# Performance work log

Hardware: AMD Instinct MI355X
Metric: run time of the kernel (lower is better)

Reference implementation:

```python
import jax, jax.numpy as jnp
import numpy as np

B, CIN, MID, COUT, H, W = 4, 256, 128, 64, 128, 128
WS, HEADS = 8, 8
HD = MID // HEADS          # head dim = 16
N = WS * WS                # tokens per window = 64


def conv2d(x, w, pad=0, groups=1):
    return jax.lax.conv_general_dilated(
        x, w, (1, 1), ((pad, pad), (pad, pad)),
        feature_group_count=groups,
        dimension_numbers=('NCHW', 'OIHW', 'NCHW'))


def bn(x, g, b):  # eval-mode BatchNorm folded to per-channel affine
    return x * g[None, :, None, None] + b[None, :, None, None]


def setup_inputs() -> dict:
    key = jax.random.key(0)
    ks = jax.random.split(key, 32)
    nrm = lambda i, sh, s: jax.random.normal(ks[i], sh, jnp.float32) * s
    return {
        'x': nrm(0, (B, CIN, H, W), 1.0),
        'conv_w': nrm(1, (MID, CIN, 3, 3), 0.03),
        'bn1_g': 1.0 + nrm(2, (MID,), 0.05), 'bn1_b': nrm(3, (MID,), 0.05),
        'qkv_w': nrm(4, (3 * MID, MID, 1, 1), 0.05),
        'loc1_w': nrm(5, (MID, MID, 3, 3), 0.03),
        'loc1_g': 1.0 + nrm(6, (MID,), 0.05), 'loc1_b': nrm(7, (MID,), 0.05),
        'loc2_w': nrm(8, (MID, MID, 1, 1), 0.05),
        'loc2_g': 1.0 + nrm(9, (MID,), 0.05), 'loc2_b': nrm(10, (MID,), 0.05),
        'rel_table': nrm(11, ((2 * WS - 1) ** 2, HEADS), 0.02),
        'cw_w': nrm(12, (1, 2, 7, 7), 0.1),
        'cw_g': 1.0 + nrm(13, (1,), 0.05), 'cw_b': nrm(14, (1,), 0.05),
        'hc_w': nrm(15, (1, 2, 7, 7), 0.1),
        'hc_g': 1.0 + nrm(16, (1,), 0.05), 'hc_b': nrm(17, (1,), 0.05),
        'hw_w': nrm(18, (1, 2, 7, 7), 0.1),
        'hw_g': 1.0 + nrm(19, (1,), 0.05), 'hw_b': nrm(20, (1,), 0.05),
        'proj_dw': nrm(21, (MID, 1, WS, WS), 0.05),
        'proj_g': 1.0 + nrm(22, (MID,), 0.05), 'proj_b': nrm(23, (MID,), 0.05),
        'proj_pw': nrm(24, (MID, MID, 1, 1), 0.05),
        'up_w': nrm(25, (COUT, MID, 3, 3), 0.03),
    }


def _rel_pos_index():
    coords = np.stack(np.meshgrid(np.arange(WS), np.arange(WS), indexing='ij')).reshape(2, -1)
    rel = (coords[:, :, None] - coords[:, None, :]).transpose(1, 2, 0) + (WS - 1)
    return (rel[:, :, 0] * (2 * WS - 1) + rel[:, :, 1]).reshape(-1)  # [N*N]


def reference(x, conv_w, bn1_g, bn1_b, qkv_w, loc1_w, loc1_g, loc1_b,
              loc2_w, loc2_g, loc2_b, rel_table, cw_w, cw_g, cw_b,
              hc_w, hc_g, hc_b, hw_w, hw_g, hw_b,
              proj_dw, proj_g, proj_b, proj_pw, up_w):
    # DecoderBlock: conv -> BN -> ReLU
    h = jax.nn.relu(bn(conv2d(x, conv_w, pad=1), bn1_g, bn1_b))  # [B,MID,H,W]

    # GlobalLocalAttention
    local = bn(conv2d(h, loc2_w), loc2_g, loc2_b) + bn(conv2d(h, loc1_w, pad=1), loc1_g, loc1_b)

    # windowed qkv (H,W divisible by WS, no pad needed)
    hh, ww = H // WS, W // WS
    qkv = conv2d(h, qkv_w)  # [B, 3*MID, H, W]
    qkv = qkv.reshape(B, 3, HEADS, HD, hh, WS, ww, WS)
    qkv = qkv.transpose(1, 0, 4, 6, 2, 5, 7, 3).reshape(3, B * hh * ww, HEADS, N, HD)
    q, k, v = qkv[0], qkv[1], qkv[2]

    dots = jnp.einsum('bhnd,bhmd->bhnm', q, k) * (HD ** -0.5)  # [Bw,HEADS,N,N]
    bias = rel_table[jnp.asarray(_rel_pos_index())].reshape(N, N, HEADS).transpose(2, 0, 1)
    dots = dots + bias[None]

    # TripletAttention on dots treated as (B', C'=HEADS, H'=N, W'=N)
    def gate(t, w, g, b):
        z = jnp.concatenate([t.max(1, keepdims=True), t.mean(1, keepdims=True)], 1)  # ZPool
        return t * jax.nn.sigmoid(bn(conv2d(z, w, pad=3), g, b))

    d1 = gate(dots.transpose(0, 2, 1, 3), cw_w, cw_g, cw_b).transpose(0, 2, 1, 3)
    d2 = gate(dots.transpose(0, 3, 2, 1), hc_w, hc_g, hc_b).transpose(0, 3, 2, 1)
    d3 = gate(dots, hw_w, hw_g, hw_b)
    dots = (d1 + d2 + d3) / 3.0

    attn = jax.nn.softmax(dots, axis=-1)
    o = jnp.einsum('bhnm,bhmd->bhnd', attn, v)
    o = o.reshape(B, hh, ww, HEADS, WS, WS, HD).transpose(0, 3, 6, 1, 4, 2, 5).reshape(B, MID, H, W)

    # avg+max pooled sigmoid gates (kernel==stride==WS//2, exact reshape pooling)
    kp = WS // 2
    aw = o.reshape(B, MID, H // kp, kp, W)
    Fw = jax.nn.sigmoid(aw.mean(3) + aw.max(3))          # [B,MID,H/4,W]
    ah = o.reshape(B, MID, H, W // kp, kp)
    Fh = jax.nn.sigmoid(ah.mean(4) + ah.max(4))          # [B,MID,H,W/4]
    gmat = jnp.einsum('bchk,bckw->bchw', Fh, Fw)         # [B,MID,H,W]

    out = o * gmat + local
    out = jnp.pad(out, ((0, 0), (0, 0), (0, 1), (0, 1)), mode='reflect')  # pad_out
    # SeparableConvBN proj: depthwise k=WS pad=3 -> BN -> 1x1
    out = conv2d(out, proj_dw, pad=3, groups=MID)
    out = conv2d(bn(out, proj_g, proj_b), proj_pw)
    out = out[:, :, :H, :W]

    # upsample: ConvTranspose2d(k=3, s=2, p=1, op=1) as dilated conv
    up = jax.lax.conv_general_dilated(
        out, up_w, (1, 1), ((1, 2), (1, 2)), lhs_dilation=(2, 2),
        dimension_numbers=('NCHW', 'OIHW', 'NCHW'))  # [B,COUT,2H,2W]
    return up
```

## Files before the change

### kernel.cpp

```cpp
#include <hip/hip_runtime.h>
#include <hip/hip_bf16.h>

typedef __hip_bfloat16 bf16;
typedef __attribute__((ext_vector_type(8))) short short8;
typedef __attribute__((ext_vector_type(4))) float f32x4;

#define DEV __device__ __forceinline__
DEV float b2f(bf16 v){ return __bfloat162float(v); }
DEV bf16 f2b(float v){ return __float2bfloat16(v); }
DEV short f2bs(float v){ union{ bf16 b; short s; } u; u.b = __float2bfloat16(v); return u.s; }
DEV float s2f(short s){ union{ short s; bf16 b; } u; u.s = s; return __bfloat162float(u.b); }
DEV float sigm(float x){ return 1.f/(1.f + expf(-x)); }

#define BB 4
#define CIN 256
#define MID 128
#define COUT 64
#define HH 128
#define WW 128
#define WS 8
#define HEADS 8
#define HD 16
#define NTOK 64
#define NWIN 1024

#define SLOT(row,cq) ((cq) ^ (((row)>>1)&3))

static const size_t OFF_H     = 0;
static const size_t OFF_LOCAL = 33554432;
static const size_t OFF_Q     = 67108864;
static const size_t OFF_K     = 83886080;
static const size_t OFF_V     = 100663296;
static const size_t OFF_DOTS  = 117440512;
static const size_t OFF_Z1    = 184549376;
static const size_t OFF_Z2    = 186646528;
static const size_t OFF_Z3    = 188743680;
static const size_t OFF_G1    = 205520896;
static const size_t OFF_G2    = 207618048;
static const size_t OFF_G3    = 209715200;
static const size_t OFF_HT    = OFF_DOTS + 34078720;

__global__ __launch_bounds__(256) void k_wrep(const float* __restrict__ w, short* __restrict__ w2){
  int i = blockIdx.x*256 + threadIdx.x;
  int ci = i & 255, co = (i >> 8) & 127, kk = i >> 15;
  w2[i] = f2bs(w[(co*256 + ci)*9 + kk]);
}

__global__ void k_xzero(short* __restrict__ xT){
  int t = blockIdx.x*256 + threadIdx.x;
  int ci = t & 255, side = (t >> 8) & 1, row = t >> 9;
  int cpad = side ? 129 : 0;
  xT[((size_t)row*130 + cpad)*256 + ci] = 0;
}

__global__ __launch_bounds__(256) void k_xrep(const float* __restrict__ x, short* __restrict__ xT){
  const int blk = blockIdx.x;
  const int cgrp = blk & 1, cig = (blk >> 1) & 7, r = (blk >> 4) & 127, b = blk >> 11;
  const int c0 = cgrp*64, ci0 = cig*32;
  __shared__ float lds[32][65];
  const int t = threadIdx.x;
  for (int i = t; i < 2048; i += 256){
    int lci = i >> 6, c = i & 63;
    lds[lci][c] = x[((size_t)(b*256 + ci0 + lci)*128 + r)*128 + c0 + c];
  }
  __syncthreads();
  for (int i = t; i < 2048; i += 256){
    int lci = i & 31, cc = i >> 5;
    xT[((size_t)(b*128 + r)*130 + c0 + cc + 1)*256 + ci0 + lci] = f2bs(lds[lci][cc]);
  }
}

__global__ __launch_bounds__(256) void k_conv1m(const short* __restrict__ xT, const short* __restrict__ w2,
      const float* __restrict__ gg, const float* __restrict__ bb, short* __restrict__ hT){
  int blk = blockIdx.x;
  blk = (blk & 7)*64 + (blk >> 3);
  const int cg = blk & 1, y2 = (blk >> 1) & 63, b = blk >> 7;
  const int t = threadIdx.x, lane = t & 63, wave = t >> 6;
  const int quad = lane >> 4, l15 = lane & 15;
  const int r = wave >> 1, x0w = (wave & 1)*64;
  __shared__ __align__(16) short smem[22784];
  short* as = smem;
  short* bs = smem + 16640;
  f32x4 acc[4][4];
  #pragma unroll
  for (int i = 0; i < 4; ++i)
    #pragma unroll
    for (int j = 0; j < 4; ++j) acc[i][j] = (f32x4){0.f,0.f,0.f,0.f};
  for (int ch = 0; ch < 8; ++ch){
    const int ci0 = ch*32;
    #pragma unroll 1
    for (int ky = 0; ky < 3; ++ky){
      __syncthreads();
      if (ky == 0){
        for (int i = t; i < 2080; i += 256){
          int sr = i / 520, j = i - sr*520;
          int col = j >> 2, cq = j & 3;
          int g = 2*y2 - 1 + sr;
          uint4 val = {0,0,0,0};
          if ((unsigned)g < 128u)
            val = *(const uint4*)&xT[((size_t)(b*128+g)*130 + col)*256 + ci0 + cq*8];
          *(uint4*)&as[((sr*130 + col)*4 + SLOT(col,cq))*8] = val;
        }
      }
      for (int i = t; i < 768; i += 256){
        int rr = i >> 2, cq = i & 3;
        int kk = ky*3 + (rr >> 6), co_l = rr & 63;
        *(uint4*)&bs[(rr*4 + SLOT(rr,cq))*8] =
          *(const uint4*)&w2[((size_t)(kk*128 + cg*64 + co_l))*256 + ci0 + cq*8];
      }
      __syncthreads();
      const int sr = r + ky;
      #pragma unroll
      for (int kx = 0; kx < 3; ++kx){
        short8 af[4], bf[4];
        #pragma unroll
        for (int mt = 0; mt < 4; ++mt){
          int col = x0w + mt*16 + l15 + kx;
          af[mt] = *(const short8*)&as[((sr*130 + col)*4 + SLOT(col,quad))*8];
        }
        #pragma unroll
        for (int nt = 0; nt < 4; ++nt){
          int rr = kx*64 + nt*16 + l15;
          bf[nt] = *(const short8*)&bs[(rr*4 + SLOT(rr,quad))*8];
        }
        #pragma unroll
        for (int mt = 0; mt < 4; ++mt)
          #pragma unroll
          for (int nt = 0; nt < 4; ++nt)
            acc[mt][nt] = __builtin_amdgcn_mfma_f32_16x16x32_bf16(af[mt], bf[nt], acc[mt][nt], 0, 0, 0);
      }
    }
  }
  __syncthreads();
  short* tb = smem;
  #pragma unroll
  for (int nt = 0; nt < 4; ++nt){
    int cl = nt*16 + l15, co = cg*64 + cl;
    float g = gg[co], bia = bb[co];
    #pragma unroll
    for (int mt = 0; mt < 4; ++mt){
      int xb = x0w + mt*16 + quad*4;
      #pragma unroll
      for (int r2 = 0; r2 < 4; ++r2)
        tb[(r*128 + xb + r2)*72 + cl] = f2bs(fmaxf(acc[mt][nt][r2]*g + bia, 0.f));
    }
  }
  __syncthreads();
  for (int i = t; i < 2048; i += 256){
    int rr = i >> 10, xx = (i >> 3) & 127, c8 = i & 7;
    *(uint4*)&hT[((size_t)(b*128 + 2*y2 + rr)*130 + xx + 1)*128 + cg*64 + c8*8] =
      *(const uint4*)&tb[(rr*128 + xx)*72 + c8*8];
  }
}

__global__ void k_hzero(short* __restrict__ hT){
  int t = blockIdx.x*256 + threadIdx.x;
  int ci = t & 127, side = (t >> 7) & 1, row = t >> 8;
  int cpad = side ? 129 : 0;
  hT[((size_t)row*130 + cpad)*128 + ci] = 0;
}

__global__ __launch_bounds__(256) void k_lwrep(const float* __restrict__ w1, const float* __restrict__ g1,
      const float* __restrict__ w2, const float* __restrict__ g2, short* __restrict__ wloc){
  int i = blockIdx.x*256 + threadIdx.x;
  int ci = i & 127, row = (i >> 7) % 384, ky = i / 49152;
  int kx = row >> 7, co = row & 127;
  float v = w1[(co*128 + ci)*9 + ky*3 + kx] * g1[co];
  if (ky == 1 && kx == 1) v += w2[co*128 + ci] * g2[co];
  wloc[i] = f2bs(v);
}

__global__ __launch_bounds__(256) void k_localm(const short* __restrict__ hT, const short* __restrict__ wloc,
      const float* __restrict__ b1, const float* __restrict__ b2, float* __restrict__ out){
  int blk = blockIdx.x;
  blk = (blk & 7)*64 + (blk >> 3);
  const int cg = blk & 1, y2 = (blk >> 1) & 63, b = blk >> 7;
  const int t = threadIdx.x, lane = t & 63, wave = t >> 6;
  const int quad = lane >> 4, l15 = lane & 15;
  const int r = wave >> 1, x0w = (wave & 1)*64;
  __shared__ __align__(16) short smem2[22784];
  short* as = smem2;
  short* bs = smem2 + 16640;
  f32x4 acc[4][4];
  #pragma unroll
  for (int i = 0; i < 4; ++i)
    #pragma unroll
    for (int j = 0; j < 4; ++j) acc[i][j] = (f32x4){0.f,0.f,0.f,0.f};
  for (int ch = 0; ch < 4; ++ch){
    const int ci0 = ch*32;
    #pragma unroll 1
    for (int ky = 0; ky < 3; ++ky){
      __syncthreads();
      if (ky == 0){
        for (int i = t; i < 2080; i += 256){
          int sr = i / 520, j = i - sr*520;
          int col = j >> 2, cq = j & 3;
          int g = 2*y2 - 1 + sr;
          uint4 val = {0,0,0,0};
          if ((unsigned)g < 128u)
            val = *(const uint4*)&hT[((size_t)(b*128+g)*130 + col)*128 + ci0 + cq*8];
          *(uint4*)&as[((sr*130 + col)*4 + SLOT(col,cq))*8] = val;
        }
      }
      for (int i = t; i < 768; i += 256){
        int rr = i >> 2, cq = i & 3;
        int kk = ky*3 + (rr >> 6), co_l = rr & 63;
        *(uint4*)&bs[(rr*4 + SLOT(rr,cq))*8] =
          *(const uint4*)&wloc[((size_t)(kk*128 + cg*64 + co_l))*128 + ci0 + cq*8];
      }
      __syncthreads();
      const int sr = r + ky;
      #pragma unroll
      for (int kx = 0; kx < 3; ++kx){
        short8 af[4], bf[4];
        #pragma unroll
        for (int mt = 0; mt < 4; ++mt){
          int col = x0w + mt*16 + l15 + kx;
          af[mt] = *(const short8*)&as[((sr*130 + col)*4 + SLOT(col,quad))*8];
        }
        #pragma unroll
        for (int nt = 0; nt < 4; ++nt){
          int rr = kx*64 + nt*16 + l15;
          bf[nt] = *(const short8*)&bs[(rr*4 + SLOT(rr,quad))*8];
        }
        #pragma unroll
        for (int mt = 0; mt < 4; ++mt)
          #pragma unroll
          for (int nt = 0; nt < 4; ++nt)
            acc[mt][nt] = __builtin_amdgcn_mfma_f32_16x16x32_bf16(af[mt], bf[nt], acc[mt][nt], 0, 0, 0);
      }
    }
  }
  const int Y = 2*y2 + r;
  #pragma unroll
  for (int nt = 0; nt < 4; ++nt){
    int co = cg*64 + nt*16 + l15;
    float bia = b1[co] + b2[co];
    #pragma unroll
    for (int mt = 0; mt < 4; ++mt){
      int xb = x0w + mt*16 + quad*4;
      float4 o4;
      o4.x = acc[mt][nt][0] + bia;
      o4.y = acc[mt][nt][1] + bia;
      o4.z = acc[mt][nt][2] + bia;
      o4.w = acc[mt][nt][3] + bia;
      *(float4*)&out[((size_t)(b*128 + co)*128 + Y)*128 + xb] = o4;
    }
  }
}

__global__ __launch_bounds__(256) void k_wqkvrep(const float* __restrict__ w, short* __restrict__ wqkv){
  int i = blockIdx.x*256 + threadIdx.x;
  wqkv[i] = f2bs(w[i]);
}

__global__ __launch_bounds__(256) void k_qkvm(const short* __restrict__ hT, const short* __restrict__ wqkv,
      bf16* __restrict__ q, bf16* __restrict__ k, bf16* __restrict__ v){
  const int blk = blockIdx.x, ocg = blockIdx.y;
  const int b = blk >> 7, y = blk & 127;
  const int t = threadIdx.x, lane = t & 63, wave = t >> 6;
  const int quad = lane >> 4, l15 = lane & 15;
  const int m0 = (wave >> 1)*64, n0 = (wave & 1)*64;
  __shared__ __align__(16) short asq[4096];
  __shared__ __align__(16) short bsq[4096];
  const short* xrow = hT + ((size_t)(b*128 + y)*130 + 1)*128;
  const short* wk   = wqkv + (size_t)ocg*128*128;
  f32x4 acc[4][4];
  #pragma unroll
  for (int i = 0; i < 4; ++i)
    #pragma unroll
    for (int j = 0; j < 4; ++j) acc[i][j] = (f32x4){0.f,0.f,0.f,0.f};
  for (int ch = 0; ch < 4; ++ch){
    const int ci0 = ch*32;
    __syncthreads();
    for (int i = t; i < 512; i += 256){
      int col = i >> 2, cq = i & 3;
      *(uint4*)&asq[(col*4 + SLOT(col,cq))*8] = *(const uint4*)&xrow[col*128 + ci0 + cq*8];
    }
    for (int i = t; i < 512; i += 256){
      int rr = i >> 2, cq = i & 3;
      *(uint4*)&bsq[(rr*4 + SLOT(rr,cq))*8] = *(const uint4*)&wk[rr*128 + ci0 + cq*8];
    }
    __syncthreads();
    short8 af[4], bf[4];
    #pragma unroll
    for (int mt = 0; mt < 4; ++mt){
      int row = m0 + mt*16 + l15;
      af[mt] = *(const short8*)&asq[(row*4 + SLOT(row,quad))*8];
    }
    #pragma unroll
    for (int nt = 0; nt < 4; ++nt){
      int row = n0 + nt*16 + l15;
      bf[nt] = *(const short8*)&bsq[(row*4 + SLOT(row,quad))*8];
    }
    #pragma unroll
    for (int mt = 0; mt < 4; ++mt)
      #pragma unroll
      for (int nt = 0; nt < 4; ++nt)
        acc[mt][nt] = __builtin_amdgcn_mfma_f32_16x16x32_bf16(af[mt], bf[nt], acc[mt][nt], 0, 0, 0);
  }
  bf16* dst = (ocg == 0) ? q : (ocg == 1) ? k : v;
  const int iy = y & 7, hy = y >> 3;
  #pragma unroll
  for (int nt = 0; nt < 4; ++nt){
    int co = n0 + nt*16 + l15;
    int head = co >> 4, d = co & 15;
    #pragma unroll
    for (int mt = 0; mt < 4; ++mt){
      int xb = m0 + mt*16 + quad*4;
      #pragma unroll
      for (int rr = 0; rr < 4; ++rr){
        int x = xb + rr;
        int bw = b*256 + hy*16 + (x >> 3);
        int n = iy*8 + (x & 7);
        dst[((size_t)(bw*8+head)*64 + n)*16 + d] = f2b(acc[mt][nt][rr]);
      }
    }
  }
}

__global__ __launch_bounds__(256) void k_dots(const bf16* __restrict__ q, const bf16* __restrict__ kk,
      const float* __restrict__ rel, bf16* __restrict__ dots){
  const int bw = blockIdx.x, hd = blockIdx.y;
  __shared__ bf16 qs[64][16], ks[64][16];
  const int t = threadIdx.x;
  const size_t base = (size_t)(bw*8+hd)*1024;
  for (int i = t; i < 1024; i += 256){ qs[i>>4][i&15] = q[base + i]; ks[i>>4][i&15] = kk[base + i]; }
  __syncthreads();
  const int n = t >> 2, jm = t & 3;
  float qr[16];
  #pragma unroll
  for (int d = 0; d < 16; ++d) qr[d] = b2f(qs[n][d]);
  const int ny = n >> 3, nx = n & 7;
  for (int mm = 0; mm < 16; ++mm){
    int m = jm*16 + mm;
    float a = 0.f;
    #pragma unroll
    for (int d = 0; d < 16; ++d) a += qr[d]*b2f(ks[m][d]);
    int my = m >> 3, mx = m & 7;
    int ridx = (ny - my + 7)*15 + (nx - mx + 7);
    float bias = rel[ridx*8 + hd];
    dots[base*4 + (size_t)n*64 + m] = f2b(a*0.25f + bias);
  }
}

__global__ __launch_bounds__(256) void k_zall(const bf16* __restrict__ dots,
      bf16* __restrict__ z1, bf16* __restrict__ z2, bf16* __restrict__ z3){
  const int bw = blockIdx.x;
  const int t = threadIdx.x;
  const int q4 = t >> 2, j4 = t & 3;
  __shared__ float sd[64][65];
  float mx3[16], sm3[16];
  #pragma unroll
  for (int i = 0; i < 16; ++i){ mx3[i] = -1e30f; sm3[i] = 0.f; }
  const short* dp = (const short*)dots + (size_t)bw*32768;
  for (int hd = 0; hd < 8; ++hd){
    __syncthreads();
    const short* p = dp + (size_t)hd*4096;
    #pragma unroll
    for (int g = 0; g < 2; ++g){
      short8 s8 = *(const short8*)&p[t*16 + g*8];
      #pragma unroll
      for (int j = 0; j < 8; ++j){
        float vv = s2f(s8[j]);
        sd[q4][j4*16 + g*8 + j] = vv;
        mx3[g*8+j] = fmaxf(mx3[g*8+j], vv);
        sm3[g*8+j] += vv;
      }
    }
    __syncthreads();
    float mx = -1e30f, sm = 0.f;
    #pragma unroll
    for (int m = 0; m < 16; ++m){
      float vv = sd[q4][j4*16 + m];
      mx = fmaxf(mx, vv); sm += vv;
    }
    mx = fmaxf(mx, __shfl_xor(mx, 1, 4));
    mx = fmaxf(mx, __shfl_xor(mx, 2, 4));
    sm += __shfl_xor(sm, 1, 4);
    sm += __shfl_xor(sm, 2, 4);
    if (j4 == 0){
      z2[(size_t)bw*1024 + q4*8 + hd]       = f2b(mx);
      z2[(size_t)bw*1024 + 512 + q4*8 + hd] = f2b(sm*(1.f/64.f));
    }
    float mxc = -1e30f, smc = 0.f;
    #pragma unroll
    for (int nn = 0; nn < 16; ++nn){
      float vv = sd[j4*16 + nn][q4];
      mxc = fmaxf(mxc, vv); smc += vv;
    }
    mxc = fmaxf(mxc, __shfl_xor(mxc, 1, 4));
    mxc = fmaxf(mxc, __shfl_xor(mxc, 2, 4));
    smc += __shfl_xor(smc, 1, 4);
    smc += __shfl_xor(smc, 2, 4);
    if (j4 == 0){
      z1[(size_t)bw*1024 + hd*64 + q4]       = f2b(mxc);
      z1[(size_t)bw*1024 + 512 + hd*64 + q4] = f2b(smc*(1.f/64.f));
    }
  }
  short* zp = (short*)z3 + (size_t)bw*8192;
  short8 o0, o1, p0, p1;
  #pragma unroll
  for (int j = 0; j < 8; ++j){
    o0[j] = f2bs(mx3[j]);        o1[j] = f2bs(mx3[8+j]);
    p0[j] = f2bs(sm3[j]*0.125f); p1[j] = f2bs(sm3[8+j]*0.125f);
  }
  *(short8*)&zp[t*16]          = o0;
  *(short8*)&zp[t*16 + 8]      = o1;
  *(short8*)&zp[4096 + t*16]   = p0;
  *(short8*)&zp[4096 + t*16+8] = p1;
}

__global__ __launch_bounds__(256) void k_gate(const bf16* __restrict__ z, const float* __restrict__ w,
      const float* __restrict__ gg, const float* __restrict__ bb, float* __restrict__ G, int R, int C){
  __shared__ float wsm[98];
  const int t = threadIdx.x;
  if (t < 98) wsm[t] = w[t];
  __syncthreads();
  const int bw = blockIdx.x;
  int p = blockIdx.y*256 + t; if (p >= R*C) return;
  int y = p / C, x = p - y*C;
  float acc = 0.f;
  for (int c = 0; c < 2; ++c)
    for (int ky = 0; ky < 7; ++ky){
      int iy = y + ky - 3; if ((unsigned)iy >= (unsigned)R) continue;
      for (int kx = 0; kx < 7; ++kx){
        int ix = x + kx - 3; if ((unsigned)ix >= (unsigned)C) continue;
        acc += b2f(z[((size_t)(bw*2+c)*R + iy)*C + ix]) * wsm[c*49 + ky*7 + kx];
      }
    }
  G[(size_t)bw*R*C + p] = sigm(acc*gg[0] + bb[0]);
}

__global__ __launch_bounds__(256) void k_gate3(const bf16* __restrict__ z, const float* __restrict__ w,
      const float* __restrict__ gg, const float* __restrict__ bb, float* __restrict__ G){
  const int bw = blockIdx.x;
  __shared__ float pad[2][70][72];
  __shared__ float wsm[98];
  const int t = threadIdx.x;
  if (t < 98) wsm[t] = w[t];
  for (int i = t; i < 2*70*70; i += 256){
    int c = i / 4900, r = i % 4900;
    int py = r / 70, px = r % 70;
    int y = py - 3, x = px - 3;
    float v = 0.f;
    if ((unsigned)y < 64u && (unsigned)x < 64u)
      v = b2f(z[(size_t)bw*8192 + c*4096 + y*64 + x]);
    pad[c][py][px] = v;
  }
  __syncthreads();
  const int tx = t & 15, ty = t >> 4;
  const int x0 = tx*4, y0 = ty*4;
  float acc[4][4] = {};
  #pragma unroll
  for (int c = 0; c < 2; ++c){
    float wr[49];
    #pragma unroll
    for (int kk = 0; kk < 49; ++kk) wr[kk] = wsm[c*49 + kk];
    #pragma unroll
    for (int iy = 0; iy < 10; ++iy){
      float row[10];
      #pragma unroll
      for (int j = 0; j < 10; ++j) row[j] = pad[c][y0+iy][x0+j];
      #pragma unroll
      for (int dy = 0; dy < 4; ++dy){
        const int ky = iy - dy;
        if (ky < 0 || ky > 6) continue;
        #pragma unroll
        for (int kx = 0; kx < 7; ++kx){
          float wv = wr[ky*7 + kx];
          #pragma unroll
          for (int dx = 0; dx < 4; ++dx)
            acc[dy][dx] += wv * row[dx + kx];
        }
      }
    }
  }
  float g0 = gg[0], b0 = bb[0];
  #pragma unroll
  for (int dy = 0; dy < 4; ++dy){
    float4 o4;
    o4.x = sigm(acc[dy][0]*g0 + b0);
    o4.y = sigm(acc[dy][1]*g0 + b0);
    o4.z = sigm(acc[dy][2]*g0 + b0);
    o4.w = sigm(acc[dy][3]*g0 + b0);
    *(float4*)&G[(size_t)bw*4096 + (y0+dy)*64 + x0] = o4;
  }
}

__global__ __launch_bounds__(256) void k_attn(const bf16* __restrict__ dots, const float* __restrict__ G1,
      const float* __restrict__ G2, const float* __restrict__ G3, const bf16* __restrict__ v,
      float* __restrict__ o){
  const int bw = blockIdx.x, hd = blockIdx.y;
  const int b = bw >> 8, wy = (bw >> 4) & 15, wx = bw & 15;
  __shared__ float attn[64][65];
  __shared__ bf16 vs[64][16];
  __shared__ float invTot[64];
  const int t = threadIdx.x;
  for (int i = t; i < 1024; i += 256) vs[i>>4][i&15] = v[(size_t)(bw*8+hd)*1024 + i];
  const int n = t >> 2, j = t & 3;
  float g2v = G2[(size_t)bw*512 + n*8 + hd];
  const bf16* dp = dots + ((size_t)(bw*8+hd)*64 + n)*64 + j*16;
  const float* g1p = G1 + (size_t)bw*512 + hd*64 + j*16;
  const float* g3p = G3 + (size_t)bw*4096 + n*64 + j*16;
  float e[16]; float mx = -1e30f;
  #pragma unroll
  for (int m = 0; m < 16; ++m){
    float dv = b2f(dp[m]) * ((g1p[m] + g2v + g3p[m]) * (1.f/3.f));
    e[m] = dv; mx = fmaxf(mx, dv);
  }
  mx = fmaxf(mx, __shfl_xor(mx, 1, 4));
  mx = fmaxf(mx, __shfl_xor(mx, 2, 4));
  float s = 0.f;
  #pragma unroll
  for (int m = 0; m < 16; ++m){ float ev = expf(e[m]-mx); e[m] = ev; s += ev; }
  s += __shfl_xor(s, 1, 4);
  s += __shfl_xor(s, 2, 4);
  #pragma unroll
  for (int m = 0; m < 16; ++m) attn[n][j*16+m] = e[m];
  if (j == 0) invTot[n] = 1.f/s;
  __syncthreads();
  const int dg = j;
  float acc[4] = {0.f,0.f,0.f,0.f};
  for (int m = 0; m < 64; ++m){
    float a = attn[n][m];
    #pragma unroll
    for (int dd = 0; dd < 4; ++dd) acc[dd] += a * b2f(vs[m][dg*4+dd]);
  }
  float it = invTot[n];
  int y = wy*8 + (n>>3), x = wx*8 + (n&7);
  #pragma unroll
  for (int dd = 0; dd < 4; ++dd){
    int c = hd*16 + dg*4 + dd;
    o[((size_t)(b*128+c)*128 + y)*128 + x] = acc[dd]*it;
  }
}

__global__ void k_fw(const float* __restrict__ o, float* __restrict__ Fw){
  int t = blockIdx.x*256 + threadIdx.x; if (t >= 4*128*32*128) return;
  int x = t & 127, kk = (t>>7) & 31, bc = t >> 12;
  const float* p = o + ((size_t)bc*128 + kk*4)*128 + x;
  float mx = -1e30f, sm = 0.f;
  #pragma unroll
  for (int r = 0; r < 4; ++r){ float v = p[r*128]; mx = fmaxf(mx,v); sm += v; }
  Fw[t] = sigm(sm*0.25f + mx);
}
__global__ void k_fh(const float* __restrict__ o, float* __restrict__ Fh){
  int t = blockIdx.x*256 + threadIdx.x; if (t >= 4*128*128*32) return;
  int kk = t & 31, y = (t>>5) & 127, bc = t >> 12;
  const float* p = o + ((size_t)bc*128 + y)*128 + kk*4;
  float mx = -1e30f, sm = 0.f;
  #pragma unroll
  for (int r = 0; r < 4; ++r){ float v = p[r]; mx = fmaxf(mx,v); sm += v; }
  Fh[t] = sigm(sm*0.25f + mx);
}

__global__ __launch_bounds__(256) void k_comb(const float* __restrict__ o, const float* __restrict__ Fh,
      const float* __restrict__ Fw, const float* __restrict__ local, float* __restrict__ comb){
  const int bc = blockIdx.x;
  __shared__ float fh[128][33];
  __shared__ float fw[32][129];
  const int t = threadIdx.x;
  for (int i = t; i < 4096; i += 256) fh[i>>5][i&31]  = Fh[(size_t)bc*4096 + i];
  for (int i = t; i < 4096; i += 256) fw[i>>7][i&127] = Fw[(size_t)bc*4096 + i];
  __syncthreads();
  for (int i = t; i < 16384; i += 256){
    int y = i >> 7, x = i & 127;
    float g = 0.f;
    #pragma unroll
    for (int kk = 0; kk < 32; ++kk) g += fh[y][kk]*fw[kk][x];
    size_t idx = (size_t)bc*16384 + i;
    comb[idx] = o[idx]*g + local[idx];
  }
}

__global__ __launch_bounds__(256) void k_dw(const float* __restrict__ comb, const float* __restrict__ dw,
      const float* __restrict__ gg, const float* __restrict__ bb, float* __restrict__ out){
  const int bz = blockIdx.y;
  const int oy0 = blockIdx.x*16;
  const int c = bz & 127;
  __shared__ float xs[23][136];
  __shared__ float wsm[64];
  const int t = threadIdx.x;
  if (t < 64) wsm[t] = dw[c*64 + t];
  for (int i = t; i < 23*135; i += 256){
    int py = i / 135, px = i - py*135;
    int gy = oy0 + py - 3, gx = px - 3;
    float v = 0.f;
    if (gy >= 0 && gy <= 128 && gx >= 0 && gx <= 128){
      int yy = (gy==128)?126:gy, xx = (gx==128)?126:gx;
      v = comb[((size_t)bz*128 + yy)*128 + xx];
    }
    xs[py][px] = v;
  }
  __syncthreads();
  const int tx = t & 31, ty = t >> 5;
  const int x0 = tx*4, y0 = ty*2;
  float acc[2][4] = {};
  #pragma unroll
  for (int iy = 0; iy < 9; ++iy){
    float row[12];
    *(float4*)&row[0] = *(const float4*)&xs[y0+iy][x0];
    *(float4*)&row[4] = *(const float4*)&xs[y0+iy][x0+4];
    *(float4*)&row[8] = *(const float4*)&xs[y0+iy][x0+8];
    #pragma unroll
    for (int dy = 0; dy < 2; ++dy){
      const int ky = iy - dy;
      if (ky < 0 || ky > 7) continue;
      #pragma unroll
      for (int kx = 0; kx < 8; ++kx){
        float wv = wsm[ky*8 + kx];
        #pragma unroll
        for (int dx = 0; dx < 4; ++dx)
          acc[dy][dx] += wv * row[dx + kx];
      }
    }
  }
  float g = gg[c], bi = bb[c];
  #pragma unroll
  for (int dy = 0; dy < 2; ++dy){
    float4 o4;
    o4.x = acc[dy][0]*g + bi;
    o4.y = acc[dy][1]*g + bi;
    o4.z = acc[dy][2]*g + bi;
    o4.w = acc[dy][3]*g + bi;
    *(float4*)&out[((size_t)bz*128 + oy0 + y0 + dy)*128 + x0] = o4;
  }
}

__global__ void k_omzero(short* __restrict__ omT){
  int t = blockIdx.x*256 + threadIdx.x;
  int ci = t & 127, side = (t >> 7) & 1, row = t >> 8;
  int cpad = side ? 129 : 0;
  omT[((size_t)row*130 + cpad)*128 + ci] = 0;
}

__global__ __launch_bounds__(256) void k_uwrep(const float* __restrict__ w, short* __restrict__ wup){
  int i = blockIdx.x*256 + threadIdx.x;
  int ci = i & 127, co = (i >> 7) & 63, tap = i >> 13;
  wup[i] = f2bs(w[(co*128 + ci)*9 + tap]);
}

__global__ __launch_bounds__(256) void k_pw(const float* __restrict__ p1, const float* __restrict__ w,
      short* __restrict__ omT){
  const int pt = blockIdx.x, cb = blockIdx.y;
  const int P0 = pt*64; const int b = P0 >> 14; const int rem0 = P0 & 16383;
  const int y = rem0 >> 7, x0 = rem0 & 127;
  __shared__ float xsm[128][65];
  __shared__ float wsm[64][129];
  const int tx = threadIdx.x, ty = threadIdx.y, t = ty*16+tx;
  for (int i = t; i < 128*64; i += 256){
    int ci = i >> 6, p = i & 63;
    xsm[ci][p] = p1[(size_t)(b*128+ci)*16384 + rem0 + p];
  }
  for (int i = t; i < 64*128; i += 256){
    int co = i >> 7, ci = i & 127;
    wsm[co][ci] = w[(cb*64+co)*128 + ci];
  }
  __syncthreads();
  float acc[4][4] = {};
  for (int ci = 0; ci < 128; ++ci){
    float hv[4], wv[4];
    #pragma unroll
    for (int jj = 0; jj < 4; ++jj) hv[jj] = xsm[ci][jj*16+tx];
    #pragma unroll
    for (int ii = 0; ii < 4; ++ii) wv[ii] = wsm[ii*16+ty][ci];
    #pragma unroll
    for (int ii = 0; ii < 4; ++ii)
      #pragma unroll
      for (int jj = 0; jj < 4; ++jj) acc[ii][jj] += wv[ii]*hv[jj];
  }
  __syncthreads();
  float* pt_t = &xsm[0][0];
  #pragma unroll
  for (int ii = 0; ii < 4; ++ii)
    #pragma unroll
    for (int jj = 0; jj < 4; ++jj)
      pt_t[(jj*16+tx)*65 + ii*16+ty] = acc[ii][jj];
  __syncthreads();
  for (int i = t; i < 4096; i += 256){
    int px = i >> 6, co_l = i & 63;
    omT[((size_t)(b*128 + y)*130 + x0 + px + 1)*128 + cb*64 + co_l] = f2bs(pt_t[px*65 + co_l]);
  }
}

__global__ __launch_bounds__(256) void k_upm(const short* __restrict__ omT, const short* __restrict__ wup,
      float* __restrict__ out){
  int blk = blockIdx.x;
  blk = (blk & 7)*64 + (blk >> 3);
  const int b = blk >> 7, y = blk & 127;
  const int t = threadIdx.x, lane = t & 63, wave = t >> 6;
  const int quad = lane >> 4, l15 = lane & 15;
  const int m0w = wave*32;
  __shared__ __align__(16) char smem[53504];
  short* asp = (short*)smem;
  short* bsp = (short*)(smem + 16640);
  float* ptile = (float*)smem;
  const int PAR[9] = {3,2,3, 1,0,1, 3,2,3};
  const int ROW[9] = {0,0,0, 0,0,0, 1,1,1};
  const int SHF[9] = {0,0,1, 0,0,1, 0,0,1};
  f32x4 acc[4][2][4];
  #pragma unroll
  for (int p = 0; p < 4; ++p)
    #pragma unroll
    for (int mt = 0; mt < 2; ++mt)
      #pragma unroll
      for (int nt = 0; nt < 4; ++nt) acc[p][mt][nt] = (f32x4){0.f,0.f,0.f,0.f};
  for (int ch = 0; ch < 4; ++ch){
    const int ci0 = ch*32;
    __syncthreads();
    for (int i = t; i < 1040; i += 256){
      int rw = (i >= 520), j = i - rw*520;
      int col = j >> 2, cq = j & 3;
      int row = rw*130 + col;
      uint4 val = {0,0,0,0};
      if (y + rw < 128)
        val = *(const uint4*)&omT[((size_t)(b*128 + y + rw)*130 + col)*128 + ci0 + cq*8];
      *(uint4*)&asp[(row*4 + SLOT(row,cq))*8] = val;
    }
    for (int i = t; i < 2304; i += 256){
      int rr = i >> 2, cq = i & 3;
      *(uint4*)&bsp[(rr*4 + SLOT(rr,cq))*8] = *(const uint4*)&wup[rr*128 + ci0 + cq*8];
    }
    __syncthreads();
    #pragma unroll
    for (int k = 0; k < 9; ++k){
      const int pr = PAR[k], rw = ROW[k], sh = SHF[k];
      if (rw && y == 127) continue;
      short8 af[2], bf[4];
      #pragma unroll
      for (int mt = 0; mt < 2; ++mt){
        int row = rw*130 + m0w + mt*16 + l15 + 1 + sh;
        af[mt] = *(const short8*)&asp[(row*4 + SLOT(row,quad))*8];
      }
      #pragma unroll
      for (int nt = 0; nt < 4; ++nt){
        int row = k*64 + nt*16 + l15;
        bf[nt] = *(const short8*)&bsp[(row*4 + SLOT(row,quad))*8];
      }
      #pragma unroll
      for (int mt = 0; mt < 2; ++mt)
        #pragma unroll
        for (int nt = 0; nt < 4; ++nt)
          acc[pr][mt][nt] = __builtin_amdgcn_mfma_f32_16x16x32_bf16(af[mt], bf[nt], acc[pr][mt][nt], 0, 0, 0);
    }
  }
  #pragma unroll
  for (int p = 0; p < 4; ++p){
    __syncthreads();
    #pragma unroll
    for (int mt = 0; mt < 2; ++mt)
      #pragma unroll
      for (int nt = 0; nt < 4; ++nt){
        int co = nt*16 + l15;
        int xb = m0w + mt*16 + quad*4;
        #pragma unroll
        for (int r = 0; r < 4; ++r)
          ptile[co*132 + xb + r] = acc[p][mt][nt][r];
      }
    __syncthreads();
    int py = p >> 1, px = p & 1;
    int Y = 2*y + py;
    for (int i = t; i < 8192; i += 256){
      int co = i >> 7, xx = i & 127;
      out[((size_t)(b*64 + co)*256 + Y)*256 + 2*xx + px] = ptile[co*132 + xx];
    }
  }
}

extern "C" void kernel_launch(void* const* d_in, const int* in_sizes, int n_in,
                              void* d_out, int out_size, void* d_ws, size_t ws_size,
                              hipStream_t stream) {
  const float* x       = (const float*)d_in[0];
  const float* conv_w  = (const float*)d_in[1];
  const float* bn1_g   = (const float*)d_in[2];
  const float* bn1_b   = (const float*)d_in[3];
  const float* qkv_w   = (const float*)d_in[4];
  const float* loc1_w  = (const float*)d_in[5];
  const float* loc1_g  = (const float*)d_in[6];
  const float* loc1_b  = (const float*)d_in[7];
  const float* loc2_w  = (const float*)d_in[8];
  const float* loc2_g  = (const float*)d_in[9];
  const float* loc2_b  = (const float*)d_in[10];
  const float* rel_t   = (const float*)d_in[11];
  const float* cw_w    = (const float*)d_in[12];
  const float* cw_g    = (const float*)d_in[13];
  const float* cw_b    = (const float*)d_in[14];
  const float* hc_w    = (const float*)d_in[15];
  const float* hc_g    = (const float*)d_in[16];
  const float* hc_b    = (const float*)d_in[17];
  const float* hw_w    = (const float*)d_in[18];
  const float* hw_g    = (const float*)d_in[19];
  const float* hw_b    = (const float*)d_in[20];
  const float* proj_dw = (const float*)d_in[21];
  const float* proj_g  = (const float*)d_in[22];
  const float* proj_b  = (const float*)d_in[23];
  const float* proj_pw = (const float*)d_in[24];
  const float* up_w    = (const float*)d_in[25];

  char* ws = (char*)d_ws;
  float* local  = (float*)(ws + OFF_LOCAL);
  bf16*  q      = (bf16*)(ws + OFF_Q);
  bf16*  k      = (bf16*)(ws + OFF_K);
  bf16*  v      = (bf16*)(ws + OFF_V);
  bf16*  dots   = (bf16*)(ws + OFF_DOTS);
  bf16*  z1     = (bf16*)(ws + OFF_Z1);
  bf16*  z2     = (bf16*)(ws + OFF_Z2);
  bf16*  z3     = (bf16*)(ws + OFF_Z3);
  float* G1     = (float*)(ws + OFF_G1);
  float* G2     = (float*)(ws + OFF_G2);
  float* G3     = (float*)(ws + OFF_G3);
  short* xT     = (short*)(ws + OFF_DOTS);
  short* hT     = (short*)(ws + OFF_HT);
  short* w2bf   = (short*)(ws + OFF_Z1);
  short* wloc   = (short*)(ws + OFF_Z2);
  short* wqkv   = (short*)(ws + OFF_Z3);
  short* omT    = (short*)(ws + OFF_DOTS);
  short* wup    = (short*)(ws + OFF_Z1);
  float* o_img  = (float*)(ws + OFF_Q);
  float* Fh     = (float*)(ws + OFF_DOTS);
  float* Fw     = (float*)(ws + OFF_DOTS + 8388608);
  float* comb   = (float*)(ws + OFF_H);
  float* proj1  = (float*)(ws + OFF_LOCAL);
  float* outp   = (float*)d_out;

  dim3 blk2(16,16);
  k_wrep <<<1152, 256, 0, stream>>>(conv_w, w2bf);
  k_xzero<<<1024, 256, 0, stream>>>(xT);
  k_xrep <<<8192, 256, 0, stream>>>(x, xT);
  k_hzero<<<512, 256, 0, stream>>>(hT);
  k_conv1m<<<512, 256, 0, stream>>>(xT, w2bf, bn1_g, bn1_b, hT);
  k_lwrep<<<576, 256, 0, stream>>>(loc1_w, loc1_g, loc2_w, loc2_g, wloc);
  k_localm<<<512, 256, 0, stream>>>(hT, wloc, loc1_b, loc2_b, local);
  k_wqkvrep<<<192, 256, 0, stream>>>(qkv_w, wqkv);
  k_qkvm <<<dim3(512,3), 256, 0, stream>>>(hT, wqkv, q, k, v);
  k_dots <<<dim3(NWIN,8), 256, 0, stream>>>(q, k, rel_t, dots);
  k_zall <<<NWIN, 256, 0, stream>>>(dots, z1, z2, z3);
  k_gate <<<dim3(NWIN,2),  256, 0, stream>>>(z1, cw_w, cw_g, cw_b, G1, 8, 64);
  k_gate <<<dim3(NWIN,2),  256, 0, stream>>>(z2, hc_w, hc_g, hc_b, G2, 64, 8);
  k_gate3<<<NWIN, 256, 0, stream>>>(z3, hw_w, hw_g, hw_b, G3);
  k_attn <<<dim3(NWIN,8), 256, 0, stream>>>(dots, G1, G2, G3, v, o_img);
  k_fw   <<<8192, 256, 0, stream>>>(o_img, Fw);
  k_fh   <<<8192, 256, 0, stream>>>(o_img, Fh);
  k_comb <<<512, 256, 0, stream>>>(o_img, Fh, Fw, local, comb);
  k_dw   <<<dim3(8, BB*128), 256, 0, stream>>>(comb, proj_dw, proj_g, proj_b, proj1);
  k_omzero<<<512, 256, 0, stream>>>(omT);
  k_uwrep<<<288, 256, 0, stream>>>(up_w, wup);
  k_pw   <<<dim3(1024,2), blk2, 0, stream>>>(proj1, proj_pw, omT);
  k_upm  <<<512, 256, 0, stream>>>(omT, wup, outp);
}
```

Baseline: 643.1 us.

## Retile 3x3 convs to 4-row blocks with register prefetch; vectorize dots and attention LDS

The two 3x3 MFMA conv kernels now use 512-thread blocks covering 4 output rows. They prefetch the next input chunk and weight slices into registers while the current slice is computed, which is meant to hide global-load latency and cut redundant halo loads. The k_dots and k_attn kernels switch to 16-byte vectorized global/LDS loads and stores, with XOR-swizzled shared layouts for k and v to avoid bank conflicts. The trade-offs are higher register and LDS use, which may lower occupancy, and half as many conv blocks.

```diff
diff --git a/kernel.cpp b/kernel.cpp
--- a/kernel.cpp
+++ b/kernel.cpp
@@ -70,86 +70,135 @@
   }
 }
 
-__global__ __launch_bounds__(256) void k_conv1m(const short* __restrict__ xT, const short* __restrict__ w2,
+__global__ __launch_bounds__(512, 2) void k_conv1m(const short* __restrict__ xT, const short* __restrict__ w2,
       const float* __restrict__ gg, const float* __restrict__ bb, short* __restrict__ hT){
   int blk = blockIdx.x;
-  blk = (blk & 7)*64 + (blk >> 3);
-  const int cg = blk & 1, y2 = (blk >> 1) & 63, b = blk >> 7;
+  blk = (blk & 7)*32 + (blk >> 3);
+  const int cg = blk & 1, y4 = (blk >> 1) & 31, b = blk >> 6;
   const int t = threadIdx.x, lane = t & 63, wave = t >> 6;
   const int quad = lane >> 4, l15 = lane & 15;
-  const int r = wave >> 1, x0w = (wave & 1)*64;
-  __shared__ __align__(16) short smem[22784];
+  const int row = wave >> 1, xh = wave & 1;
+  const int x0w = xh*64;
+  __shared__ __align__(16) short smem[31104];
   short* as = smem;
-  short* bs = smem + 16640;
+  short* bs = smem + 24960;
+  uint4 areg[7], breg[2];
   f32x4 acc[4][4];
   #pragma unroll
   for (int i = 0; i < 4; ++i)
     #pragma unroll
     for (int j = 0; j < 4; ++j) acc[i][j] = (f32x4){0.f,0.f,0.f,0.f};
+
+  auto loadA = [&](int ch){
+    const int ci0 = ch*32;
+    #pragma unroll
+    for (int j = 0; j < 7; ++j){
+      int i = t + j*512;
+      uint4 val = {0,0,0,0};
+      if (j < 6 || i < 3120){
+        int sr = i / 520, jj = i - sr*520;
+        int col = jj >> 2, cq = jj & 3;
+        int g = y4*4 - 1 + sr;
+        if ((unsigned)g < 128u)
+          val = *(const uint4*)&xT[((size_t)(b*128+g)*130 + col)*256 + ci0 + cq*8];
+      }
+      areg[j] = val;
+    }
+  };
+  auto writeA = [&](){
+    #pragma unroll
+    for (int j = 0; j < 7; ++j){
+      int i = t + j*512;
+      if (j == 6 && i >= 3120) break;
+      int sr = i / 520, jj = i - sr*520;
+      int col = jj >> 2, cq = jj & 3;
+      *(uint4*)&as[((sr*130 + col)*4 + SLOT(col,cq))*8] = areg[j];
+    }
+  };
+  auto loadB = [&](int ch, int ky){
+    const int ci0 = ch*32;
+    #pragma unroll
+    for (int j = 0; j < 2; ++j){
+      int i = t + j*512;
+      if (j == 1 && t >= 256) break;
+      int rr = i >> 2, cq = i & 3;
+      int kk = ky*3 + (rr >> 6), co_l = rr & 63;
+      breg[j] = *(const uint4*)&w2[((size_t)(kk*128 + cg*64 + co_l))*256 + ci0 + cq*8];
+    }
+  };
+  auto writeB = [&](){
+    #pragma unroll
+    for (int j = 0; j < 2; ++j){
+      int i = t + j*512;
+      if (j == 1 && t >= 256) break;
+      int rr = i >> 2, cq = i & 3;
+      *(uint4*)&bs[(rr*4 + SLOT(rr,cq))*8] = breg[j];
+    }
+  };
+  auto compute = [&](int sr){
+    #pragma unroll
+    for (int kx = 0; kx < 3; ++kx){
+      short8 af[4], bf[4];
+      #pragma unroll
+      for (int mt = 0; mt < 4; ++mt){
+        int col = x0w + mt*16 + l15 + kx;
+        af[mt] = *(const short8*)&as[((sr*130 + col)*4 + SLOT(col,quad))*8];
+      }
+      #pragma unroll
+      for (int nt = 0; nt < 4; ++nt){
+        int rr = kx*64 + nt*16 + l15;
+        bf[nt] = *(const short8*)&bs[(rr*4 + SLOT(rr,quad))*8];
+      }
+      #pragma unroll
+      for (int mt = 0; mt < 4; ++mt)
+        #pragma unroll
+        for (int nt = 0; nt < 4; ++nt)
+          acc[mt][nt] = __builtin_amdgcn_mfma_f32_16x16x32_bf16(af[mt], bf[nt], acc[mt][nt], 0, 0, 0);
+    }
+  };
+
+  loadA(0); loadB(0, 0);
+  #pragma unroll 1
   for (int ch = 0; ch < 8; ++ch){
-    const int ci0 = ch*32;
-    #pragma unroll 1
-    for (int ky = 0; ky < 3; ++ky){
-      __syncthreads();
-      if (ky == 0){
-        for (int i = t; i < 2080; i += 256){
-          int sr = i / 520, j = i - sr*520;
-          int col = j >> 2, cq = j & 3;
-          int g = 2*y2 - 1 + sr;
-          uint4 val = {0,0,0,0};
-          if ((unsigned)g < 128u)
-            val = *(const uint4*)&xT[((size_t)(b*128+g)*130 + col)*256 + ci0 + cq*8];
-          *(uint4*)&as[((sr*130 + col)*4 + SLOT(col,cq))*8] = val;
-        }
-      }
-      for (int i = t; i < 768; i += 256){
-        int rr = i >> 2, cq = i & 3;
-        int kk = ky*3 + (rr >> 6), co_l = rr & 63;
-        *(uint4*)&bs[(rr*4 + SLOT(rr,cq))*8] =
-          *(const uint4*)&w2[((size_t)(kk*128 + cg*64 + co_l))*256 + ci0 + cq*8];
-      }
-      __syncthreads();
-      const int sr = r + ky;
-      #pragma unroll
-      for (int kx = 0; kx < 3; ++kx){
-        short8 af[4], bf[4];
+    __syncthreads();
+    writeA(); writeB();
+    loadB(ch, 1);
+    __syncthreads();
+    compute(row + 0);
+    __syncthreads();
+    writeB(); loadB(ch, 2);
+    __syncthreads();
+    compute(row + 1);
+    __syncthreads();
+    writeB();
+    if (ch < 7){ loadA(ch+1); loadB(ch+1, 0); }
+    __syncthreads();
+    compute(row + 2);
+  }
+  short* tb = smem;
+  #pragma unroll 1
+  for (int p = 0; p < 2; ++p){
+    __syncthreads();
+    if ((row >> 1) == p){
+      #pragma unroll
+      for (int nt = 0; nt < 4; ++nt){
+        int cl = nt*16 + l15, co = cg*64 + cl;
+        float g = gg[co], bia = bb[co];
         #pragma unroll
         for (int mt = 0; mt < 4; ++mt){
-          int col = x0w + mt*16 + l15 + kx;
-          af[mt] = *(const short8*)&as[((sr*130 + col)*4 + SLOT(col,quad))*8];
+          int xb = x0w + mt*16 + quad*4;
+          #pragma unroll
+          for (int r2 = 0; r2 < 4; ++r2)
+            tb[((row & 1)*128 + xb + r2)*72 + cl] = f2bs(fmaxf(acc[mt][nt][r2]*g + bia, 0.f));
         }
-        #pragma unroll
-        for (int nt = 0; nt < 4; ++nt){
-          int rr = kx*64 + nt*16 + l15;
-          bf[nt] = *(const short8*)&bs[(rr*4 + SLOT(rr,quad))*8];
-        }
-        #pragma unroll
-        for (int mt = 0; mt < 4; ++mt)
-          #pragma unroll
-          for (int nt = 0; nt < 4; ++nt)
-            acc[mt][nt] = __builtin_amdgcn_mfma_f32_16x16x32_bf16(af[mt], bf[nt], acc[mt][nt], 0, 0, 0);
-      }
-    }
-  }
-  __syncthreads();
-  short* tb = smem;
-  #pragma unroll
-  for (int nt = 0; nt < 4; ++nt){
-    int cl = nt*16 + l15, co = cg*64 + cl;
-    float g = gg[co], bia = bb[co];
-    #pragma unroll
-    for (int mt = 0; mt < 4; ++mt){
-      int xb = x0w + mt*16 + quad*4;
-      #pragma unroll
-      for (int r2 = 0; r2 < 4; ++r2)
-        tb[(r*128 + xb + r2)*72 + cl] = f2bs(fmaxf(acc[mt][nt][r2]*g + bia, 0.f));
-    }
-  }
-  __syncthreads();
-  for (int i = t; i < 2048; i += 256){
-    int rr = i >> 10, xx = (i >> 3) & 127, c8 = i & 7;
-    *(uint4*)&hT[((size_t)(b*128 + 2*y2 + rr)*130 + xx + 1)*128 + cg*64 + c8*8] =
-      *(const uint4*)&tb[(rr*128 + xx)*72 + c8*8];
+      }
+    }
+    __syncthreads();
+    for (int i = t; i < 2048; i += 512){
+      int rr = i >> 10, xx = (i >> 3) & 127, c8 = i & 7;
+      *(uint4*)&hT[((size_t)(b*128 + y4*4 + p*2 + rr)*130 + xx + 1)*128 + cg*64 + c8*8] =
+        *(const uint4*)&tb[(rr*128 + xx)*72 + c8*8];
+    }
   }
 }
 
@@ -170,68 +219,112 @@
   wloc[i] = f2bs(v);
 }
 
-__global__ __launch_bounds__(256) void k_localm(const short* __restrict__ hT, const short* __restrict__ wloc,
+__global__ __launch_bounds__(512, 2) void k_localm(const short* __restrict__ hT, const short* __restrict__ wloc,
       const float* __restrict__ b1, const float* __restrict__ b2, float* __restrict__ out){
   int blk = blockIdx.x;
-  blk = (blk & 7)*64 + (blk >> 3);
-  const int cg = blk & 1, y2 = (blk >> 1) & 63, b = blk >> 7;
+  blk = (blk & 7)*32 + (blk >> 3);
+  const int cg = blk & 1, y4 = (blk >> 1) & 31, b = blk >> 6;
   const int t = threadIdx.x, lane = t & 63, wave = t >> 6;
   const int quad = lane >> 4, l15 = lane & 15;
-  const int r = wave >> 1, x0w = (wave & 1)*64;
-  __shared__ __align__(16) short smem2[22784];
+  const int row = wave >> 1, xh = wave & 1;
+  const int x0w = xh*64;
+  __shared__ __align__(16) short smem2[31104];
   short* as = smem2;
-  short* bs = smem2 + 16640;
+  short* bs = smem2 + 24960;
+  uint4 areg[7], breg[2];
   f32x4 acc[4][4];
   #pragma unroll
   for (int i = 0; i < 4; ++i)
     #pragma unroll
     for (int j = 0; j < 4; ++j) acc[i][j] = (f32x4){0.f,0.f,0.f,0.f};
+
+  auto loadA = [&](int ch){
+    const int ci0 = ch*32;
+    #pragma unroll
+    for (int j = 0; j < 7; ++j){
+      int i = t + j*512;
+      uint4 val = {0,0,0,0};
+      if (j < 6 || i < 3120){
+        int sr = i / 520, jj = i - sr*520;
+        int col = jj >> 2, cq = jj & 3;
+        int g = y4*4 - 1 + sr;
+        if ((unsigned)g < 128u)
+          val = *(const uint4*)&hT[((size_t)(b*128+g)*130 + col)*128 + ci0 + cq*8];
+      }
+      areg[j] = val;
+    }
+  };
+  auto writeA = [&](){
+    #pragma unroll
+    for (int j = 0; j < 7; ++j){
+      int i = t + j*512;
+      if (j == 6 && i >= 3120) break;
+      int sr = i / 520, jj = i - sr*520;
+      int col = jj >> 2, cq = jj & 3;
+      *(uint4*)&as[((sr*130 + col)*4 + SLOT(col,cq))*8] = areg[j];
+    }
+  };
+  auto loadB = [&](int ch, int ky){
+    const int ci0 = ch*32;
+    #pragma unroll
+    for (int j = 0; j < 2; ++j){
+      int i = t + j*512;
+      if (j == 1 && t >= 256) break;
+      int rr = i >> 2, cq = i & 3;
+      int kk = ky*3 + (rr >> 6), co_l = rr & 63;
+      breg[j] = *(const uint4*)&wloc[((size_t)(kk*128 + cg*64 + co_l))*128 + ci0 + cq*8];
+    }
+  };
+  auto writeB = [&](){
+    #pragma unroll
+    for (int j = 0; j < 2; ++j){
+      int i = t + j*512;
+      if (j == 1 && t >= 256) break;
+      int rr = i >> 2, cq = i & 3;
+      *(uint4*)&bs[(rr*4 + SLOT(rr,cq))*8] = breg[j];
+    }
+  };
+  auto compute = [&](int sr){
+    #pragma unroll
+    for (int kx = 0; kx < 3; ++kx){
+      short8 af[4], bf[4];
+      #pragma unroll
+      for (int mt = 0; mt < 4; ++mt){
+        int col = x0w + mt*16 + l15 + kx;
+        af[mt] = *(const short8*)&as[((sr*130 + col)*4 + SLOT(col,quad))*8];
+      }
+      #pragma unroll
+      for (int nt = 0; nt < 4; ++nt){
+        int rr = kx*64 + nt*16 + l15;
+        bf[nt] = *(const short8*)&bs[(rr*4 + SLOT(rr,quad))*8];
+      }
+      #pragma unroll
+      for (int mt = 0; mt < 4; ++mt)
+        #pragma unroll
+        for (int nt = 0; nt < 4; ++nt)
+          acc[mt][nt] = __builtin_amdgcn_mfma_f32_16x16x32_bf16(af[mt], bf[nt], acc[mt][nt], 0, 0, 0);
+    }
+  };
+
+  loadA(0); loadB(0, 0);
+  #pragma unroll 1
   for (int ch = 0; ch < 4; ++ch){
-    const int ci0 = ch*32;
-    #pragma unroll 1
-    for (int ky = 0; ky < 3; ++ky){
-      __syncthreads();
-      if (ky == 0){
-        for (int i = t; i < 2080; i += 256){
-          int sr = i / 520, j = i - sr*520;
-          int col = j >> 2, cq = j & 3;
-          int g = 2*y2 - 1 + sr;
-          uint4 val = {0,0,0,0};
-          if ((unsigned)g < 128u)
-            val = *(const uint4*)&hT[((size_t)(b*128+g)*130 + col)*128 + ci0 + cq*8];
-          *(uint4*)&as[((sr*130 + col)*4 + SLOT(col,cq))*8] = val;
-        }
-      }
-      for (int i = t; i < 768; i += 256){
-        int rr = i >> 2, cq = i & 3;
-        int kk = ky*3 + (rr >> 6), co_l = rr & 63;
-        *(uint4*)&bs[(rr*4 + SLOT(rr,cq))*8] =
-          *(const uint4*)&wloc[((size_t)(kk*128 + cg*64 + co_l))*128 + ci0 + cq*8];
-      }
-      __syncthreads();
-      const int sr = r + ky;
-      #pragma unroll
-      for (int kx = 0; kx < 3; ++kx){
-        short8 af[4], bf[4];
-        #pragma unroll
-        for (int mt = 0; mt < 4; ++mt){
-          int col = x0w + mt*16 + l15 + kx;
-          af[mt] = *(const short8*)&as[((sr*130 + col)*4 + SLOT(col,quad))*8];
-        }
-        #pragma unroll
-        for (int nt = 0; nt < 4; ++nt){
-          int rr = kx*64 + nt*16 + l15;
-          bf[nt] = *(const short8*)&bs[(rr*4 + SLOT(rr,quad))*8];
-        }
-        #pragma unroll
-        for (int mt = 0; mt < 4; ++mt)
-          #pragma unroll
-          for (int nt = 0; nt < 4; ++nt)
-            acc[mt][nt] = __builtin_amdgcn_mfma_f32_16x16x32_bf16(af[mt], bf[nt], acc[mt][nt], 0, 0, 0);
-      }
-    }
-  }
-  const int Y = 2*y2 + r;
+    __syncthreads();
+    writeA(); writeB();
+    loadB(ch, 1);
+    __syncthreads();
+    compute(row + 0);
+    __syncthreads();
+    writeB(); loadB(ch, 2);
+    __syncthreads();
+    compute(row + 1);
+    __syncthreads();
+    writeB();
+    if (ch < 3){ loadA(ch+1); loadB(ch+1, 0); }
+    __syncthreads();
+    compute(row + 2);
+  }
+  const int Y = y4*4 + row;
   #pragma unroll
   for (int nt = 0; nt < 4; ++nt){
     int co = cg*64 + nt*16 + l15;
@@ -322,26 +415,53 @@
 __global__ __launch_bounds__(256) void k_dots(const bf16* __restrict__ q, const bf16* __restrict__ kk,
       const float* __restrict__ rel, bf16* __restrict__ dots){
   const int bw = blockIdx.x, hd = blockIdx.y;
-  __shared__ bf16 qs[64][16], ks[64][16];
+  __shared__ __align__(16) short qs[64][16];
+  __shared__ __align__(16) short ks2[64][16];
   const int t = threadIdx.x;
   const size_t base = (size_t)(bw*8+hd)*1024;
-  for (int i = t; i < 1024; i += 256){ qs[i>>4][i&15] = q[base + i]; ks[i>>4][i&15] = kk[base + i]; }
+  const short* qp = (const short*)q;
+  const short* kp = (const short*)kk;
+  if (t < 64){
+    *(uint4*)&qs[t][0] = *(const uint4*)&qp[base + t*16];
+    *(uint4*)&qs[t][8] = *(const uint4*)&qp[base + t*16 + 8];
+  } else if (t < 128){
+    int r = t - 64;
+    uint4 a0 = *(const uint4*)&kp[base + r*16];
+    uint4 a1 = *(const uint4*)&kp[base + r*16 + 8];
+    int p = (r >> 4) & 1;
+    *(uint4*)&ks2[r][p*8]     = a0;
+    *(uint4*)&ks2[r][8 - p*8] = a1;
+  }
   __syncthreads();
   const int n = t >> 2, jm = t & 3;
   float qr[16];
-  #pragma unroll
-  for (int d = 0; d < 16; ++d) qr[d] = b2f(qs[n][d]);
+  short8 q0 = *(const short8*)&qs[n][0];
+  short8 q1 = *(const short8*)&qs[n][8];
+  #pragma unroll
+  for (int d = 0; d < 8; ++d){ qr[d] = s2f(q0[d]); qr[8+d] = s2f(q1[d]); }
   const int ny = n >> 3, nx = n & 7;
+  float a[16];
+  #pragma unroll
   for (int mm = 0; mm < 16; ++mm){
     int m = jm*16 + mm;
-    float a = 0.f;
-    #pragma unroll
-    for (int d = 0; d < 16; ++d) a += qr[d]*b2f(ks[m][d]);
+    int p = (m >> 4) & 1;
+    short8 k0 = *(const short8*)&ks2[m][p*8];
+    short8 k1 = *(const short8*)&ks2[m][8 - p*8];
+    float acc = 0.f;
+    #pragma unroll
+    for (int d = 0; d < 8; ++d) acc += qr[d]*s2f(k0[d]);
+    #pragma unroll
+    for (int d = 0; d < 8; ++d) acc += qr[8+d]*s2f(k1[d]);
     int my = m >> 3, mx = m & 7;
     int ridx = (ny - my + 7)*15 + (nx - mx + 7);
-    float bias = rel[ridx*8 + hd];
-    dots[base*4 + (size_t)n*64 + m] = f2b(a*0.25f + bias);
-  }
+    a[mm] = acc*0.25f + rel[ridx*8 + hd];
+  }
+  short8 s0, s1;
+  #pragma unroll
+  for (int j = 0; j < 8; ++j){ s0[j] = f2bs(a[j]); s1[j] = f2bs(a[8+j]); }
+  short* dp = (short*)dots + base*4 + (size_t)n*64 + jm*16;
+  *(short8*)&dp[0] = s0;
+  *(short8*)&dp[8] = s1;
 }
 
 __global__ __launch_bounds__(256) void k_zall(const bf16* __restrict__ dots,
@@ -493,20 +613,27 @@
       float* __restrict__ o){
   const int bw = blockIdx.x, hd = blockIdx.y;
   const int b = bw >> 8, wy = (bw >> 4) & 15, wx = bw & 15;
-  __shared__ float attn[64][65];
-  __shared__ bf16 vs[64][16];
+  __shared__ __align__(16) float attn[64][68];
+  __shared__ __align__(16) short vst2[16][64];
   __shared__ float invTot[64];
   const int t = threadIdx.x;
-  for (int i = t; i < 1024; i += 256) vs[i>>4][i&15] = v[(size_t)(bw*8+hd)*1024 + i];
+  const short* vp = (const short*)v;
+  for (int i = t; i < 1024; i += 256){
+    int m = i >> 4, d = i & 15;
+    int oo = m >> 3, rr = m & 7;
+    vst2[d][((oo ^ (d >> 2)) << 3) + rr] = vp[(size_t)(bw*8+hd)*1024 + i];
+  }
   const int n = t >> 2, j = t & 3;
   float g2v = G2[(size_t)bw*512 + n*8 + hd];
-  const bf16* dp = dots + ((size_t)(bw*8+hd)*64 + n)*64 + j*16;
+  const short* dp = (const short*)dots + ((size_t)(bw*8+hd)*64 + n)*64 + j*16;
   const float* g1p = G1 + (size_t)bw*512 + hd*64 + j*16;
   const float* g3p = G3 + (size_t)bw*4096 + n*64 + j*16;
+  short8 d0 = *(const short8*)&dp[0];
+  short8 d1 = *(const short8*)&dp[8];
   float e[16]; float mx = -1e30f;
   #pragma unroll
   for (int m = 0; m < 16; ++m){
-    float dv = b2f(dp[m]) * ((g1p[m] + g2v + g3p[m]) * (1.f/3.f));
+    float dv = s2f(m < 8 ? d0[m] : d1[m-8]) * ((g1p[m] + g2v + g3p[m]) * (1.f/3.f));
     e[m] = dv; mx = fmaxf(mx, dv);
   }
   mx = fmaxf(mx, __shfl_xor(mx, 1, 4));
@@ -520,19 +647,24 @@
   for (int m = 0; m < 16; ++m) attn[n][j*16+m] = e[m];
   if (j == 0) invTot[n] = 1.f/s;
   __syncthreads();
-  const int dg = j;
-  float acc[4] = {0.f,0.f,0.f,0.f};
-  for (int m = 0; m < 64; ++m){
-    float a = attn[n][m];
-    #pragma unroll
-    for (int dd = 0; dd < 4; ++dd) acc[dd] += a * b2f(vs[m][dg*4+dd]);
+  float acc4[4] = {0.f,0.f,0.f,0.f};
+  #pragma unroll
+  for (int oo = 0; oo < 8; ++oo){
+    float4 a0 = *(const float4*)&attn[n][oo*8];
+    float4 a1 = *(const float4*)&attn[n][oo*8+4];
+    #pragma unroll
+    for (int dd = 0; dd < 4; ++dd){
+      short8 v8 = *(const short8*)&vst2[j*4+dd][((oo ^ j) << 3)];
+      acc4[dd] += a0.x*s2f(v8[0]) + a0.y*s2f(v8[1]) + a0.z*s2f(v8[2]) + a0.w*s2f(v8[3])
+                + a1.x*s2f(v8[4]) + a1.y*s2f(v8[5]) + a1.z*s2f(v8[6]) + a1.w*s2f(v8[7]);
+    }
   }
   float it = invTot[n];
   int y = wy*8 + (n>>3), x = wx*8 + (n&7);
   #pragma unroll
   for (int dd = 0; dd < 4; ++dd){
-    int c = hd*16 + dg*4 + dd;
-    o[((size_t)(b*128+c)*128 + y)*128 + x] = acc[dd]*it;
+    int c = hd*16 + j*4 + dd;
+    o[((size_t)(b*128+c)*128 + y)*128 + x] = acc4[dd]*it;
   }
 }
 
@@ -829,9 +961,9 @@
   k_xzero<<<1024, 256, 0, stream>>>(xT);
   k_xrep <<<8192, 256, 0, stream>>>(x, xT);
   k_hzero<<<512, 256, 0, stream>>>(hT);
-  k_conv1m<<<512, 256, 0, stream>>>(xT, w2bf, bn1_g, bn1_b, hT);
+  k_conv1m<<<256, 512, 0, stream>>>(xT, w2bf, bn1_g, bn1_b, hT);
   k_lwrep<<<576, 256, 0, stream>>>(loc1_w, loc1_g, loc2_w, loc2_g, wloc);
-  k_localm<<<512, 256, 0, stream>>>(hT, wloc, loc1_b, loc2_b, local);
+  k_localm<<<256, 512, 0, stream>>>(hT, wloc, loc1_b, loc2_b, local);
   k_wqkvrep<<<192, 256, 0, stream>>>(qkv_w, wqkv);
   k_qkvm <<<dim3(512,3), 256, 0, stream>>>(hT, wqkv, q, k, v);
   k_dots <<<dim3(NWIN,8), 256, 0, stream>>>(q, k, rel_t, dots);
```

New measurement: 665.0 us. +3.4%, slower.
